# Optimization experiments

Hardware: AMD Instinct MI355X
Metric: run time of the kernel (lower is better)

Reference implementation:

```python
import jax, jax.numpy as jnp
import numpy as np

B, T, HID = 2, 2048, 2048
NH, NKV, HD = 16, 4, 128
GROUPS = NH // NKV

def _rotate_half(t):
    t1, t2 = jnp.split(t, 2, axis=-1)
    return jnp.concatenate([-t2, t1], axis=-1)

def _apply_rotary(t, cos, sin):
    # t: [B, H, T, D], cos/sin: [1, 1, T, D]
    return t * cos + _rotate_half(t) * sin

def setup_inputs() -> dict:
    key = jax.random.key(0)
    ks = jax.random.split(key, 6)
    x = jax.random.normal(ks[0], (B, T, HID), dtype=jnp.float32)
    # real rotary tables
    inv_freq = 1.0 / (10000.0 ** (jnp.arange(0, HD, 2, dtype=jnp.float32) / HD))
    pos = jnp.arange(T, dtype=jnp.float32)
    freqs = jnp.outer(pos, inv_freq)            # [T, D/2]
    emb = jnp.concatenate([freqs, freqs], -1)   # [T, D]
    cos = jnp.cos(emb)[None, None]              # [1,1,T,D]
    sin = jnp.sin(emb)[None, None]
    s = 0.02
    Wq = jax.random.normal(ks[1], (HID, NH * HD), dtype=jnp.float32) * s
    Wk = jax.random.normal(ks[2], (HID, NKV * HD), dtype=jnp.float32) * s
    Wv = jax.random.normal(ks[3], (HID, NKV * HD), dtype=jnp.float32) * s
    Wo = jax.random.normal(ks[4], (NH * HD, HID), dtype=jnp.float32) * s
    return {"x": x, "cos": cos, "sin": sin, "Wq": Wq, "Wk": Wk, "Wv": Wv, "Wo": Wo}

def reference(x, cos, sin, Wq, Wk, Wv, Wo):
    b, t, _ = x.shape
    q = (x @ Wq).reshape(b, t, NH, HD).transpose(0, 2, 1, 3)    # [B,NH,T,D]
    k = (x @ Wk).reshape(b, t, NKV, HD).transpose(0, 2, 1, 3)   # [B,NKV,T,D]
    v = (x @ Wv).reshape(b, t, NKV, HD).transpose(0, 2, 1, 3)
    q = _apply_rotary(q, cos, sin)
    k = _apply_rotary(k, cos, sin)
    # GQA without repeat_interleave: group q-heads by kv-head
    qg = q.reshape(b, NKV, GROUPS, t, HD)                       # [B,KV,G,T,D]
    scale = 1.0 / jnp.sqrt(jnp.float32(HD))
    scores = jnp.einsum('bkgtd,bksd->bkgts', qg, k) * scale     # [B,KV,G,T,S]
    causal = jnp.tril(jnp.ones((t, t), dtype=bool))
    scores = jnp.where(causal[None, None, None], scores, jnp.float32(-1e30))
    attn = jax.nn.softmax(scores, axis=-1)
    out = jnp.einsum('bkgts,bksd->bkgtd', attn, v)              # [B,KV,G,T,D]
    out = out.reshape(b, NH, t, HD).transpose(0, 2, 1, 3).reshape(b, t, NH * HD)
    return out @ Wo
```

## Files before the change

kernel.cpp:

```cpp
#include <hip/hip_runtime.h>
#include <hip/hip_bf16.h>
#include <cstdint>

typedef unsigned short u16;
typedef unsigned int u32;
typedef __bf16 bf16x8 __attribute__((ext_vector_type(8)));
typedef float f32x4 __attribute__((ext_vector_type(4)));

#define BDIM 2
#define TDIM 2048
#define HIDDIM 2048
#define NHEAD 16
#define NKVH 4
#define HD 128
#define MROWS (BDIM*TDIM)
#define NQKV 3072
#define KDIM 2048

#define MFMA16(a,b,c) __builtin_amdgcn_mfma_f32_16x16x32_bf16((a),(b),(c),0,0,0)

__device__ __forceinline__ u16 f2bf(float f) {
    __bf16 h = (__bf16)f;
    return __builtin_bit_cast(u16, h);
}
__device__ __forceinline__ float bf2f(u32 u) {
    u <<= 16;
    return __builtin_bit_cast(float, u);
}
__device__ __forceinline__ void gld16(const void* g, void* l) {
    __builtin_amdgcn_global_load_lds(
        (const __attribute__((address_space(1))) u32*)g,
        (__attribute__((address_space(3))) u32*)l, 16, 0, 0);
}

__global__ __launch_bounds__(256) void prep_kernel(const float* __restrict__ x,
                                                   u16* __restrict__ xb,
                                                   const float* __restrict__ Wq,
                                                   const float* __restrict__ Wk,
                                                   const float* __restrict__ Wv,
                                                   const float* __restrict__ Wo,
                                                   u16* __restrict__ Wqkvt,
                                                   u16* __restrict__ Wot) {
    __shared__ float tile[32][33];
    const int bi = blockIdx.x;
    const int tid = threadIdx.x;
    if (bi < 4096) {
        size_t i = ((size_t)bi * 256 + tid) * 8;
        float4 a = *(const float4*)(x + i);
        float4 b = *(const float4*)(x + i + 4);
        uint4 v;
        v.x = (u32)f2bf(a.x) | ((u32)f2bf(a.y) << 16);
        v.y = (u32)f2bf(a.z) | ((u32)f2bf(a.w) << 16);
        v.z = (u32)f2bf(b.x) | ((u32)f2bf(b.y) << 16);
        v.w = (u32)f2bf(b.z) | ((u32)f2bf(b.w) << 16);
        *(uint4*)(xb + i) = v;
        return;
    }
    const float* src;
    u16* dst;
    int N, n0, k0;
    if (bi < 8192) {
        int t = bi - 4096; src = Wq; dst = Wqkvt; N = 2048;
        n0 = (t & 63) * 32; k0 = (t >> 6) * 32;
    } else if (bi < 9216) {
        int t = bi - 8192; src = Wk; dst = Wqkvt + (size_t)2048 * KDIM; N = 512;
        n0 = (t & 15) * 32; k0 = (t >> 4) * 32;
    } else if (bi < 10240) {
        int t = bi - 9216; src = Wv; dst = Wqkvt + (size_t)2560 * KDIM; N = 512;
        n0 = (t & 15) * 32; k0 = (t >> 4) * 32;
    } else {
        int t = bi - 10240; src = Wo; dst = Wot; N = 2048;
        n0 = (t & 63) * 32; k0 = (t >> 6) * 32;
    }
    const int tx = tid & 31, ty = tid >> 5;
#pragma unroll
    for (int r = 0; r < 4; r++)
        tile[ty + 8*r][tx] = src[(size_t)(k0 + ty + 8*r) * N + n0 + tx];
    __syncthreads();
#pragma unroll
    for (int r = 0; r < 4; r++)
        dst[(size_t)(n0 + ty + 8*r) * KDIM + k0 + tx] = f2bf(tile[tx][ty + 8*r]);
}

template<int OUT_BF16>
__global__ void __launch_bounds__(256, 2) gemm_bt(const u16* __restrict__ A,
                                                  const u16* __restrict__ Bt,
                                                  void* __restrict__ C, int ldc) {
    __shared__ __align__(16) u16 Al[128 * 32];
    __shared__ __align__(16) u16 Bl[128 * 32];
    const int tid = threadIdx.x;
    const int lane = tid & 63;
    const int w = tid >> 6;
    const int wm = (w & 1) * 64;
    const int wn = (w >> 1) * 64;
    const int quad = lane >> 4;
    const int l15 = lane & 15;
    const size_t bm = (size_t)blockIdx.x * 128;
    const size_t bn = (size_t)blockIdx.y * 128;

    const int srow = lane >> 2;
    const int kq = (lane & 3) ^ ((lane >> 3) & 3);
    const int i0 = 2 * w, i1 = 2 * w + 1;

    const u16* ga0 = A + (bm + i0*16 + srow) * KDIM + kq * 8;
    const u16* ga1 = A + (bm + i1*16 + srow) * KDIM + kq * 8;
    const u16* gb0 = Bt + (bn + i0*16 + srow) * KDIM + kq * 8;
    const u16* gb1 = Bt + (bn + i1*16 + srow) * KDIM + kq * 8;

    const int swz = ((quad ^ ((l15 >> 1) & 3)) << 3);
    int aoff[4], boff[4];
#pragma unroll
    for (int t = 0; t < 4; t++) {
        aoff[t] = (wm + t*16 + l15) * 32 + swz;
        boff[t] = (wn + t*16 + l15) * 32 + swz;
    }

    f32x4 acc[4][4] = {};

    for (int kt = 0; kt < KDIM / 32; kt++) {
        gld16(ga0 + kt*32, &Al[i0 * 512]);
        gld16(ga1 + kt*32, &Al[i1 * 512]);
        gld16(gb0 + kt*32, &Bl[i0 * 512]);
        gld16(gb1 + kt*32, &Bl[i1 * 512]);
        __syncthreads();
        bf16x8 af[4], bfv[4];
#pragma unroll
        for (int t = 0; t < 4; t++) {
            af[t]  = *(const bf16x8*)&Al[aoff[t]];
            bfv[t] = *(const bf16x8*)&Bl[boff[t]];
        }
#pragma unroll
        for (int mt = 0; mt < 4; mt++)
#pragma unroll
            for (int nt = 0; nt < 4; nt++)
                acc[mt][nt] = MFMA16(af[mt], bfv[nt], acc[mt][nt]);
        __syncthreads();
    }

#pragma unroll
    for (int mt = 0; mt < 4; mt++) {
        size_t m0 = bm + wm + mt*16 + quad*4;
#pragma unroll
        for (int nt = 0; nt < 4; nt++) {
            size_t n = bn + wn + nt*16 + l15;
#pragma unroll
            for (int r = 0; r < 4; r++) {
                if (OUT_BF16)
                    ((u16*)C)[(m0 + r) * (size_t)ldc + n] = f2bf(acc[mt][nt][r]);
                else
                    ((float*)C)[(m0 + r) * (size_t)ldc + n] = acc[mt][nt][r];
            }
        }
    }
}

__global__ __launch_bounds__(256) void rotary_kernel(u16* __restrict__ QKV,
                                                     const float* __restrict__ cosT,
                                                     const float* __restrict__ sinT) {
    int i = blockIdx.x * 256 + threadIdx.x;
    int m = i / 320;
    int rem = i - m * 320;
    int head = rem >> 4;
    int d0 = (rem & 15) << 2;
    int t = m & (TDIM - 1);
    int col;
    float sc;
    if (head < NHEAD) {
        col = head * HD + d0;
        sc = 0.08838834764831845f * 1.4426950408889634f;
    } else {
        col = HIDDIM + (head - NHEAD) * HD + d0;
        sc = 1.0f;
    }
    u16* p0 = QKV + (size_t)m * NQKV + col;
    u16* p1 = p0 + 64;
    float4 cv = *(const float4*)(cosT + t * HD + d0);
    float4 sv = *(const float4*)(sinT + t * HD + d0);
    uint2 qa = *(const uint2*)p0;
    uint2 qb = *(const uint2*)p1;
    float f0[4] = { bf2f(qa.x & 0xffffu), bf2f(qa.x >> 16), bf2f(qa.y & 0xffffu), bf2f(qa.y >> 16) };
    float f1[4] = { bf2f(qb.x & 0xffffu), bf2f(qb.x >> 16), bf2f(qb.y & 0xffffu), bf2f(qb.y >> 16) };
    float c[4] = { cv.x, cv.y, cv.z, cv.w };
    float s[4] = { sv.x, sv.y, sv.z, sv.w };
    u16 o0[4], o1[4];
#pragma unroll
    for (int k = 0; k < 4; k++) {
        o0[k] = f2bf((f0[k] * c[k] - f1[k] * s[k]) * sc);
        o1[k] = f2bf((f1[k] * c[k] + f0[k] * s[k]) * sc);
    }
    uint2 w0, w1;
    w0.x = (u32)o0[0] | ((u32)o0[1] << 16);
    w0.y = (u32)o0[2] | ((u32)o0[3] << 16);
    w1.x = (u32)o1[0] | ((u32)o1[1] << 16);
    w1.y = (u32)o1[2] | ((u32)o1[3] << 16);
    *(uint2*)p0 = w0;
    *(uint2*)p1 = w1;
}

__global__ void __launch_bounds__(256, 2) attn_kernel(const u16* __restrict__ QKV,
                                                      u16* __restrict__ AO) {
    constexpr int LV = 72;
    __shared__ __align__(16) u16 Kl[2][64 * 128];
    __shared__ __align__(16) u16 Vt[128 * LV];

    const int pa = blockIdx.x;
    const int h  = blockIdx.y;
    const int b  = blockIdx.z;
    const int kh = h >> 2;
    const int tid = threadIdx.x;
    const int lane = tid & 63;
    const int w = tid >> 6;
    const int quad = lane >> 4;
    const int l15 = lane & 15;

    const size_t rowbase = (size_t)b * TDIM;
    const u16* Qb = QKV + rowbase * NQKV + h * HD;
    const u16* Kb = QKV + rowbase * NQKV + HIDDIM + kh * HD;
    const u16* Vb = Kb + NKVH * HD;

    int krow[4], kgch[4];
#pragma unroll
    for (int i = 0; i < 4; i++) {
        krow[i] = w*16 + i*4 + quad;
        kgch[i] = l15 ^ (krow[i] & 7);
    }
    const int sp0 = tid & 31, dch0 = tid >> 5, dch1 = dch0 + 8;
    const int s0v = sp0 * 2;
    const int ccv = (s0v & ~0x1C) | ((s0v & 0x0C) << 1) | ((s0v & 0x10) >> 2);

#pragma unroll 1
    for (int ph = 0; ph < 2; ph++) {
        const int qt = ph ? (31 - pa) : pa;

        bf16x8 qf[4];
        {
            const u16* qr = Qb + (size_t)(qt*64 + w*16 + l15) * NQKV;
#pragma unroll
            for (int kt = 0; kt < 4; kt++)
                qf[kt] = *(const bf16x8*)(qr + kt*32 + quad*8);
        }
        f32x4 O[8] = {};
        float mrun = -1e30f, lrun = 0.0f;

#pragma unroll
        for (int i = 0; i < 4; i++)
            gld16(Kb + (size_t)krow[i] * NQKV + kgch[i]*8, &Kl[0][(w*16 + i*4) * 128]);
        uint4 vr0a, vr0b, vr1a, vr1b;
        {
            const u16* g0 = Vb + (size_t)s0v * NQKV + dch0*8;
            vr0a = *(const uint4*)g0;
            vr0b = *(const uint4*)(g0 + NQKV);
            const u16* g1 = Vb + (size_t)s0v * NQKV + dch1*8;
            vr1a = *(const uint4*)g1;
            vr1b = *(const uint4*)(g1 + NQKV);
        }

#pragma unroll 1
        for (int j = 0; j <= qt; j++) {
            {
                u32 ra[4] = { vr0a.x, vr0a.y, vr0a.z, vr0a.w };
                u32 rb[4] = { vr0b.x, vr0b.y, vr0b.z, vr0b.w };
                int d0 = dch0*8;
#pragma unroll
                for (int k2 = 0; k2 < 4; k2++) {
                    u32 lo = (ra[k2] & 0xffffu) | (rb[k2] << 16);
                    u32 hi = (ra[k2] >> 16) | (rb[k2] & 0xffff0000u);
                    *(u32*)&Vt[(d0 + 2*k2)     * LV + ccv] = lo;
                    *(u32*)&Vt[(d0 + 2*k2 + 1) * LV + ccv] = hi;
                }
                u32 rc[4] = { vr1a.x, vr1a.y, vr1a.z, vr1a.w };
                u32 rd[4] = { vr1b.x, vr1b.y, vr1b.z, vr1b.w };
                d0 = dch1*8;
#pragma unroll
                for (int k2 = 0; k2 < 4; k2++) {
                    u32 lo = (rc[k2] & 0xffffu) | (rd[k2] << 16);
                    u32 hi = (rc[k2] >> 16) | (rd[k2] & 0xffff0000u);
                    *(u32*)&Vt[(d0 + 2*k2)     * LV + ccv] = lo;
                    *(u32*)&Vt[(d0 + 2*k2 + 1) * LV + ccv] = hi;
                }
            }
            __syncthreads();

            if (j < qt) {
                const u16* Kbn = Kb + (size_t)(j+1) * 64 * NQKV;
                u16* kl = Kl[(j+1) & 1];
#pragma unroll
                for (int i = 0; i < 4; i++)
                    gld16(Kbn + (size_t)krow[i] * NQKV + kgch[i]*8, &kl[(w*16 + i*4) * 128]);
                const u16* Vbn = Vb + (size_t)(j+1) * 64 * NQKV;
                const u16* g0 = Vbn + (size_t)s0v * NQKV + dch0*8;
                vr0a = *(const uint4*)g0;
                vr0b = *(const uint4*)(g0 + NQKV);
                const u16* g1 = Vbn + (size_t)s0v * NQKV + dch1*8;
                vr1a = *(const uint4*)g1;
                vr1b = *(const uint4*)(g1 + NQKV);
            }

            const u16* kl = Kl[j & 1];
            f32x4 S[4] = {};
            __builtin_amdgcn_s_setprio(1);
#pragma unroll
            for (int kt = 0; kt < 4; kt++) {
                int p = (kt*4 + quad) ^ (l15 & 7);
#pragma unroll
                for (int nt = 0; nt < 4; nt++) {
                    bf16x8 afr = *(const bf16x8*)&kl[(nt*16 + l15)*128 + p*8];
                    S[nt] = MFMA16(afr, qf[kt], S[nt]);
                }
            }
            __builtin_amdgcn_s_setprio(0);

            if (j == qt) {
                const int qloc = w*16 + l15;
#pragma unroll
                for (int nt = 0; nt < 4; nt++) {
                    const int sb = nt*16 + quad*4;
#pragma unroll
                    for (int r = 0; r < 4; r++)
                        if (sb + r > qloc) S[nt][r] = -1e30f;
                }
            }

            bool grow;
            {
                float mx0 = fmaxf(fmaxf(S[0][0], S[0][1]), fmaxf(S[0][2], S[0][3]));
                float mx1 = fmaxf(fmaxf(S[1][0], S[1][1]), fmaxf(S[1][2], S[1][3]));
                float mx2 = fmaxf(fmaxf(S[2][0], S[2][1]), fmaxf(S[2][2], S[2][3]));
                float mx3 = fmaxf(fmaxf(S[3][0], S[3][1]), fmaxf(S[3][2], S[3][3]));
                float mx = fmaxf(fmaxf(mx0, mx1), fmaxf(mx2, mx3));
                mx = fmaxf(mx, __shfl_xor(mx, 16, 64));
                mx = fmaxf(mx, __shfl_xor(mx, 32, 64));
                grow = __any(mx > mrun + 8.0f);
                float alpha = 1.0f;
                if (grow) {
                    float mnew = fmaxf(mrun, mx);
                    alpha = __builtin_amdgcn_exp2f(mrun - mnew);
                    mrun = mnew;
                }
                float rs = 0.0f;
#pragma unroll
                for (int nt = 0; nt < 4; nt++)
#pragma unroll
                    for (int r = 0; r < 4; r++) {
                        float pv = __builtin_amdgcn_exp2f(S[nt][r] - mrun);
                        S[nt][r] = pv;
                        rs += pv;
                    }
                rs += __shfl_xor(rs, 16, 64);
                rs += __shfl_xor(rs, 32, 64);
                lrun = lrun * alpha + rs;
                if (grow) {
#pragma unroll
                    for (int nt = 0; nt < 8; nt++)
                        O[nt] *= alpha;
                }
            }

            u32 c0[4], c1[4];
#pragma unroll
            for (int nt = 0; nt < 4; nt++) {
                c0[nt] = (u32)f2bf(S[nt][0]) | ((u32)f2bf(S[nt][1]) << 16);
                c1[nt] = (u32)f2bf(S[nt][2]) | ((u32)f2bf(S[nt][3]) << 16);
            }
            __builtin_amdgcn_s_setprio(1);
#pragma unroll
            for (int kt = 0; kt < 2; kt++) {
                uint4 bq;
                bq.x = c0[2*kt];
                bq.y = c1[2*kt];
                bq.z = c0[2*kt+1];
                bq.w = c1[2*kt+1];
                bf16x8 pf = __builtin_bit_cast(bf16x8, bq);
#pragma unroll
                for (int nt = 0; nt < 8; nt++) {
                    bf16x8 av = *(const bf16x8*)&Vt[(nt*16 + l15) * LV + kt*32 + quad*8];
                    O[nt] = MFMA16(av, pf, O[nt]);
                }
            }
            __builtin_amdgcn_s_setprio(0);
            __syncthreads();
        }

        {
            float inv = 1.0f / lrun;
            size_t row = rowbase + qt*64 + w*16 + l15;
            u16* outp = AO + row * HIDDIM + h * HD + quad*4;
#pragma unroll
            for (int nt = 0; nt < 8; nt++) {
                uint2 o;
                o.x = (u32)f2bf(O[nt][0] * inv) | ((u32)f2bf(O[nt][1] * inv) << 16);
                o.y = (u32)f2bf(O[nt][2] * inv) | ((u32)f2bf(O[nt][3] * inv) << 16);
                *(uint2*)(outp + nt*16) = o;
            }
        }
    }
}

extern "C" void kernel_launch(void* const* d_in, const int* in_sizes, int n_in,
                              void* d_out, int out_size, void* d_ws, size_t ws_size,
                              hipStream_t stream) {
    (void)in_sizes; (void)n_in; (void)out_size; (void)ws_size;
    const float* x    = (const float*)d_in[0];
    const float* cosT = (const float*)d_in[1];
    const float* sinT = (const float*)d_in[2];
    const float* Wq   = (const float*)d_in[3];
    const float* Wk   = (const float*)d_in[4];
    const float* Wv   = (const float*)d_in[5];
    const float* Wo   = (const float*)d_in[6];

    char* ws = (char*)d_ws;
    u16* QKV   = (u16*)ws;
    u16* xb    = (u16*)(ws + (size_t)MROWS * NQKV * 2);
    u16* Wqkvt = (u16*)(ws + (size_t)MROWS * NQKV * 2 + (size_t)MROWS * HIDDIM * 2);
    u16* Wot   = Wqkvt + (size_t)NQKV * KDIM;

    prep_kernel<<<14336, 256, 0, stream>>>(x, xb, Wq, Wk, Wv, Wo, Wqkvt, Wot);
    gemm_bt<1><<<dim3(32, 24), 256, 0, stream>>>(xb, Wqkvt, QKV, NQKV);
    rotary_kernel<<<5120, 256, 0, stream>>>(QKV, cosT, sinT);
    attn_kernel<<<dim3(16, 16, 2), 256, 0, stream>>>(QKV, xb);
    gemm_bt<0><<<dim3(32, 16), 256, 0, stream>>>(xb, Wot, d_out, HIDDIM);
}
```

Baseline: 307.2 us.

## Double-buffer transposed V tile to drop one barrier per KV iteration

The transposed V tile in shared memory becomes double-buffered. The next tile's transpose-and-store now happens after the P·V MFMAs of the current tile rather than at the top of the next iteration. This removes the trailing __syncthreads per KV step, leaving one barrier per iteration, and lets the V scatter overlap other waves' compute. It costs an extra 18KB of LDS, which may reduce occupancy under the 2-blocks-per-CU launch bound. It also requires the K/V prefetch ordering to stay correct with only a single barrier.

```diff
diff --git a/kernel.cpp b/kernel.cpp
--- a/kernel.cpp
+++ b/kernel.cpp
@@ -201,7 +201,7 @@
                                                       u16* __restrict__ AO) {
     constexpr int LV = 72;
     __shared__ __align__(16) u16 Kl[2][64 * 128];
-    __shared__ __align__(16) u16 Vt[128 * LV];
+    __shared__ __align__(16) u16 Vt[2][128 * LV];
 
     const int pa = blockIdx.x;
     const int h  = blockIdx.y;
@@ -242,9 +242,8 @@
         f32x4 O[8] = {};
         float mrun = -1e30f, lrun = 0.0f;
 
-#pragma unroll
-        for (int i = 0; i < 4; i++)
-            gld16(Kb + (size_t)krow[i] * NQKV + kgch[i]*8, &Kl[0][(w*16 + i*4) * 128]);
+        __syncthreads();
+
         uint4 vr0a, vr0b, vr1a, vr1b;
         {
             const u16* g0 = Vb + (size_t)s0v * NQKV + dch0*8;
@@ -254,39 +253,38 @@
             vr1a = *(const uint4*)g1;
             vr1b = *(const uint4*)(g1 + NQKV);
         }
+#pragma unroll
+        for (int i = 0; i < 4; i++)
+            gld16(Kb + (size_t)krow[i] * NQKV + kgch[i]*8, &Kl[0][(w*16 + i*4) * 128]);
+        {
+            u16* vt = &Vt[0][0];
+            u32 ra[4] = { vr0a.x, vr0a.y, vr0a.z, vr0a.w };
+            u32 rb[4] = { vr0b.x, vr0b.y, vr0b.z, vr0b.w };
+            int d0 = dch0*8;
+#pragma unroll
+            for (int k2 = 0; k2 < 4; k2++) {
+                u32 lo = (ra[k2] & 0xffffu) | (rb[k2] << 16);
+                u32 hi = (ra[k2] >> 16) | (rb[k2] & 0xffff0000u);
+                *(u32*)&vt[(d0 + 2*k2)     * LV + ccv] = lo;
+                *(u32*)&vt[(d0 + 2*k2 + 1) * LV + ccv] = hi;
+            }
+            u32 rc[4] = { vr1a.x, vr1a.y, vr1a.z, vr1a.w };
+            u32 rd[4] = { vr1b.x, vr1b.y, vr1b.z, vr1b.w };
+            d0 = dch1*8;
+#pragma unroll
+            for (int k2 = 0; k2 < 4; k2++) {
+                u32 lo = (rc[k2] & 0xffffu) | (rd[k2] << 16);
+                u32 hi = (rc[k2] >> 16) | (rd[k2] & 0xffff0000u);
+                *(u32*)&vt[(d0 + 2*k2)     * LV + ccv] = lo;
+                *(u32*)&vt[(d0 + 2*k2 + 1) * LV + ccv] = hi;
+            }
+        }
 
 #pragma unroll 1
         for (int j = 0; j <= qt; j++) {
-            {
-                u32 ra[4] = { vr0a.x, vr0a.y, vr0a.z, vr0a.w };
-                u32 rb[4] = { vr0b.x, vr0b.y, vr0b.z, vr0b.w };
-                int d0 = dch0*8;
-#pragma unroll
-                for (int k2 = 0; k2 < 4; k2++) {
-                    u32 lo = (ra[k2] & 0xffffu) | (rb[k2] << 16);
-                    u32 hi = (ra[k2] >> 16) | (rb[k2] & 0xffff0000u);
-                    *(u32*)&Vt[(d0 + 2*k2)     * LV + ccv] = lo;
-                    *(u32*)&Vt[(d0 + 2*k2 + 1) * LV + ccv] = hi;
-                }
-                u32 rc[4] = { vr1a.x, vr1a.y, vr1a.z, vr1a.w };
-                u32 rd[4] = { vr1b.x, vr1b.y, vr1b.z, vr1b.w };
-                d0 = dch1*8;
-#pragma unroll
-                for (int k2 = 0; k2 < 4; k2++) {
-                    u32 lo = (rc[k2] & 0xffffu) | (rd[k2] << 16);
-                    u32 hi = (rc[k2] >> 16) | (rd[k2] & 0xffff0000u);
-                    *(u32*)&Vt[(d0 + 2*k2)     * LV + ccv] = lo;
-                    *(u32*)&Vt[(d0 + 2*k2 + 1) * LV + ccv] = hi;
-                }
-            }
             __syncthreads();
 
             if (j < qt) {
-                const u16* Kbn = Kb + (size_t)(j+1) * 64 * NQKV;
-                u16* kl = Kl[(j+1) & 1];
-#pragma unroll
-                for (int i = 0; i < 4; i++)
-                    gld16(Kbn + (size_t)krow[i] * NQKV + kgch[i]*8, &kl[(w*16 + i*4) * 128]);
                 const u16* Vbn = Vb + (size_t)(j+1) * 64 * NQKV;
                 const u16* g0 = Vbn + (size_t)s0v * NQKV + dch0*8;
                 vr0a = *(const uint4*)g0;
@@ -294,9 +292,14 @@
                 const u16* g1 = Vbn + (size_t)s0v * NQKV + dch1*8;
                 vr1a = *(const uint4*)g1;
                 vr1b = *(const uint4*)(g1 + NQKV);
-            }
-
-            const u16* kl = Kl[j & 1];
+                const u16* Kbn = Kb + (size_t)(j+1) * 64 * NQKV;
+                u16* kl = &Kl[(j+1) & 1][0];
+#pragma unroll
+                for (int i = 0; i < 4; i++)
+                    gld16(Kbn + (size_t)krow[i] * NQKV + kgch[i]*8, &kl[(w*16 + i*4) * 128]);
+            }
+
+            const u16* kl = &Kl[j & 1][0];
             f32x4 S[4] = {};
             __builtin_amdgcn_s_setprio(1);
 #pragma unroll
@@ -362,6 +365,7 @@
                 c0[nt] = (u32)f2bf(S[nt][0]) | ((u32)f2bf(S[nt][1]) << 16);
                 c1[nt] = (u32)f2bf(S[nt][2]) | ((u32)f2bf(S[nt][3]) << 16);
             }
+            const u16* vt = &Vt[j & 1][0];
             __builtin_amdgcn_s_setprio(1);
 #pragma unroll
             for (int kt = 0; kt < 2; kt++) {
@@ -373,12 +377,35 @@
                 bf16x8 pf = __builtin_bit_cast(bf16x8, bq);
 #pragma unroll
                 for (int nt = 0; nt < 8; nt++) {
-                    bf16x8 av = *(const bf16x8*)&Vt[(nt*16 + l15) * LV + kt*32 + quad*8];
+                    bf16x8 av = *(const bf16x8*)&vt[(nt*16 + l15) * LV + kt*32 + quad*8];
                     O[nt] = MFMA16(av, pf, O[nt]);
                 }
             }
             __builtin_amdgcn_s_setprio(0);
-            __syncthreads();
+
+            if (j < qt) {
+                u16* vtn = &Vt[(j+1) & 1][0];
+                u32 ra[4] = { vr0a.x, vr0a.y, vr0a.z, vr0a.w };
+                u32 rb[4] = { vr0b.x, vr0b.y, vr0b.z, vr0b.w };
+                int d0 = dch0*8;
+#pragma unroll
+                for (int k2 = 0; k2 < 4; k2++) {
+                    u32 lo = (ra[k2] & 0xffffu) | (rb[k2] << 16);
+                    u32 hi = (ra[k2] >> 16) | (rb[k2] & 0xffff0000u);
+                    *(u32*)&vtn[(d0 + 2*k2)     * LV + ccv] = lo;
+                    *(u32*)&vtn[(d0 + 2*k2 + 1) * LV + ccv] = hi;
+                }
+                u32 rc[4] = { vr1a.x, vr1a.y, vr1a.z, vr1a.w };
+                u32 rd[4] = { vr1b.x, vr1b.y, vr1b.z, vr1b.w };
+                d0 = dch1*8;
+#pragma unroll
+                for (int k2 = 0; k2 < 4; k2++) {
+                    u32 lo = (rc[k2] & 0xffffu) | (rd[k2] << 16);
+                    u32 hi = (rc[k2] >> 16) | (rd[k2] & 0xffff0000u);
+                    *(u32*)&vtn[(d0 + 2*k2)     * LV + ccv] = lo;
+                    *(u32*)&vtn[(d0 + 2*k2 + 1) * LV + ccv] = hi;
+                }
+            }
         }
 
         {
```

Measured after the change: 303.4 us. Within noise of the previous version (-1.2%).

## Process 128 query rows per attention block, reusing K/V tiles across two sub-tiles

Applied to the files above, without the earlier changes.

Each attention block now handles a 128-row query tile (two 16-row sub-tiles per wave) instead of two paired 64-row tiles, so every K/V tile staged in shared memory feeds twice as many MFMAs. The grid becomes a flat 512-block launch, ordered so that long and short causal tiles are interleaved for load balance. This is meant to halve K/V global loads and the V transpose work per query row and to raise MFMA density. In exchange, register pressure roughly doubles for the accumulators and Q fragments, which may reduce occupancy, and per-block work becomes more uneven.

```diff
diff --git a/kernel.cpp b/kernel.cpp
--- a/kernel.cpp
+++ b/kernel.cpp
@@ -203,9 +203,14 @@
     __shared__ __align__(16) u16 Kl[2][64 * 128];
     __shared__ __align__(16) u16 Vt[128 * LV];
 
-    const int pa = blockIdx.x;
-    const int h  = blockIdx.y;
-    const int b  = blockIdx.z;
+    const int l  = blockIdx.x;
+    const int cc = l & 255;
+    const int pq = cc & 7;
+    const int h  = (cc >> 3) & 15;
+    const int b  = cc >> 7;
+    const int qt = (l >> 8) ? (15 - pq) : pq;
+    const int nj = 2 * qt + 2;
+
     const int kh = h >> 2;
     const int tid = threadIdx.x;
     const int lane = tid & 63;
@@ -228,170 +233,188 @@
     const int s0v = sp0 * 2;
     const int ccv = (s0v & ~0x1C) | ((s0v & 0x0C) << 1) | ((s0v & 0x10) >> 2);
 
+    bf16x8 qf[2][4];
+#pragma unroll
+    for (int mi = 0; mi < 2; mi++) {
+        const u16* qr = Qb + (size_t)(qt*128 + w*32 + mi*16 + l15) * NQKV;
+#pragma unroll
+        for (int kt = 0; kt < 4; kt++)
+            qf[mi][kt] = *(const bf16x8*)(qr + kt*32 + quad*8);
+    }
+    f32x4 O[2][8] = {};
+    float mrun[2] = { -1e30f, -1e30f }, lrun[2] = { 0.0f, 0.0f };
+
+#pragma unroll
+    for (int i = 0; i < 4; i++)
+        gld16(Kb + (size_t)krow[i] * NQKV + kgch[i]*8, &Kl[0][(w*16 + i*4) * 128]);
+    uint4 vr0a, vr0b, vr1a, vr1b;
+    {
+        const u16* g0 = Vb + (size_t)s0v * NQKV + dch0*8;
+        vr0a = *(const uint4*)g0;
+        vr0b = *(const uint4*)(g0 + NQKV);
+        const u16* g1 = Vb + (size_t)s0v * NQKV + dch1*8;
+        vr1a = *(const uint4*)g1;
+        vr1b = *(const uint4*)(g1 + NQKV);
+    }
+
 #pragma unroll 1
-    for (int ph = 0; ph < 2; ph++) {
-        const int qt = ph ? (31 - pa) : pa;
-
-        bf16x8 qf[4];
+    for (int j = 0; j < nj; j++) {
         {
-            const u16* qr = Qb + (size_t)(qt*64 + w*16 + l15) * NQKV;
-#pragma unroll
-            for (int kt = 0; kt < 4; kt++)
-                qf[kt] = *(const bf16x8*)(qr + kt*32 + quad*8);
-        }
-        f32x4 O[8] = {};
-        float mrun = -1e30f, lrun = 0.0f;
-
-#pragma unroll
-        for (int i = 0; i < 4; i++)
-            gld16(Kb + (size_t)krow[i] * NQKV + kgch[i]*8, &Kl[0][(w*16 + i*4) * 128]);
-        uint4 vr0a, vr0b, vr1a, vr1b;
-        {
-            const u16* g0 = Vb + (size_t)s0v * NQKV + dch0*8;
+            u32 ra[4] = { vr0a.x, vr0a.y, vr0a.z, vr0a.w };
+            u32 rb[4] = { vr0b.x, vr0b.y, vr0b.z, vr0b.w };
+            int d0 = dch0*8;
+#pragma unroll
+            for (int k2 = 0; k2 < 4; k2++) {
+                u32 lo = (ra[k2] & 0xffffu) | (rb[k2] << 16);
+                u32 hi = (ra[k2] >> 16) | (rb[k2] & 0xffff0000u);
+                *(u32*)&Vt[(d0 + 2*k2)     * LV + ccv] = lo;
+                *(u32*)&Vt[(d0 + 2*k2 + 1) * LV + ccv] = hi;
+            }
+            u32 rc[4] = { vr1a.x, vr1a.y, vr1a.z, vr1a.w };
+            u32 rd[4] = { vr1b.x, vr1b.y, vr1b.z, vr1b.w };
+            d0 = dch1*8;
+#pragma unroll
+            for (int k2 = 0; k2 < 4; k2++) {
+                u32 lo = (rc[k2] & 0xffffu) | (rd[k2] << 16);
+                u32 hi = (rc[k2] >> 16) | (rd[k2] & 0xffff0000u);
+                *(u32*)&Vt[(d0 + 2*k2)     * LV + ccv] = lo;
+                *(u32*)&Vt[(d0 + 2*k2 + 1) * LV + ccv] = hi;
+            }
+        }
+        __syncthreads();
+
+        if (j + 1 < nj) {
+            const u16* Kbn = Kb + (size_t)(j+1) * 64 * NQKV;
+            u16* kl = &Kl[(j+1) & 1][0];
+#pragma unroll
+            for (int i = 0; i < 4; i++)
+                gld16(Kbn + (size_t)krow[i] * NQKV + kgch[i]*8, &kl[(w*16 + i*4) * 128]);
+            const u16* Vbn = Vb + (size_t)(j+1) * 64 * NQKV;
+            const u16* g0 = Vbn + (size_t)s0v * NQKV + dch0*8;
             vr0a = *(const uint4*)g0;
             vr0b = *(const uint4*)(g0 + NQKV);
-            const u16* g1 = Vb + (size_t)s0v * NQKV + dch1*8;
+            const u16* g1 = Vbn + (size_t)s0v * NQKV + dch1*8;
             vr1a = *(const uint4*)g1;
             vr1b = *(const uint4*)(g1 + NQKV);
         }
 
-#pragma unroll 1
-        for (int j = 0; j <= qt; j++) {
-            {
-                u32 ra[4] = { vr0a.x, vr0a.y, vr0a.z, vr0a.w };
-                u32 rb[4] = { vr0b.x, vr0b.y, vr0b.z, vr0b.w };
-                int d0 = dch0*8;
-#pragma unroll
-                for (int k2 = 0; k2 < 4; k2++) {
-                    u32 lo = (ra[k2] & 0xffffu) | (rb[k2] << 16);
-                    u32 hi = (ra[k2] >> 16) | (rb[k2] & 0xffff0000u);
-                    *(u32*)&Vt[(d0 + 2*k2)     * LV + ccv] = lo;
-                    *(u32*)&Vt[(d0 + 2*k2 + 1) * LV + ccv] = hi;
+        const u16* kl = &Kl[j & 1][0];
+        f32x4 S[2][4] = {};
+        __builtin_amdgcn_s_setprio(1);
+#pragma unroll
+        for (int kt = 0; kt < 4; kt++) {
+            int p = (kt*4 + quad) ^ (l15 & 7);
+#pragma unroll
+            for (int nt = 0; nt < 4; nt++) {
+                bf16x8 afr = *(const bf16x8*)&kl[(nt*16 + l15)*128 + p*8];
+                S[0][nt] = MFMA16(afr, qf[0][kt], S[0][nt]);
+                S[1][nt] = MFMA16(afr, qf[1][kt], S[1][nt]);
+            }
+        }
+        __builtin_amdgcn_s_setprio(0);
+
+        if (j >= 2*qt) {
+            const int sb0 = (j - 2*qt) * 64;
+#pragma unroll
+            for (int mi = 0; mi < 2; mi++) {
+                const int qloc = w*32 + mi*16 + l15;
+#pragma unroll
+                for (int nt = 0; nt < 4; nt++) {
+                    const int sb = sb0 + nt*16 + quad*4;
+#pragma unroll
+                    for (int r = 0; r < 4; r++)
+                        if (sb + r > qloc) S[mi][nt][r] = -1e30f;
                 }
-                u32 rc[4] = { vr1a.x, vr1a.y, vr1a.z, vr1a.w };
-                u32 rd[4] = { vr1b.x, vr1b.y, vr1b.z, vr1b.w };
-                d0 = dch1*8;
-#pragma unroll
-                for (int k2 = 0; k2 < 4; k2++) {
-                    u32 lo = (rc[k2] & 0xffffu) | (rd[k2] << 16);
-                    u32 hi = (rc[k2] >> 16) | (rd[k2] & 0xffff0000u);
-                    *(u32*)&Vt[(d0 + 2*k2)     * LV + ccv] = lo;
-                    *(u32*)&Vt[(d0 + 2*k2 + 1) * LV + ccv] = hi;
+            }
+        }
+
+        {
+            float mx[2];
+#pragma unroll
+            for (int mi = 0; mi < 2; mi++) {
+                float a0 = fmaxf(fmaxf(S[mi][0][0], S[mi][0][1]), fmaxf(S[mi][0][2], S[mi][0][3]));
+                float a1 = fmaxf(fmaxf(S[mi][1][0], S[mi][1][1]), fmaxf(S[mi][1][2], S[mi][1][3]));
+                float a2 = fmaxf(fmaxf(S[mi][2][0], S[mi][2][1]), fmaxf(S[mi][2][2], S[mi][2][3]));
+                float a3 = fmaxf(fmaxf(S[mi][3][0], S[mi][3][1]), fmaxf(S[mi][3][2], S[mi][3][3]));
+                float m = fmaxf(fmaxf(a0, a1), fmaxf(a2, a3));
+                m = fmaxf(m, __shfl_xor(m, 16, 64));
+                m = fmaxf(m, __shfl_xor(m, 32, 64));
+                mx[mi] = m;
+            }
+            bool grow = __any((mx[0] > mrun[0] + 8.0f) | (mx[1] > mrun[1] + 8.0f));
+            float alpha[2] = { 1.0f, 1.0f };
+            if (grow) {
+#pragma unroll
+                for (int mi = 0; mi < 2; mi++) {
+                    float mn = fmaxf(mrun[mi], mx[mi]);
+                    alpha[mi] = __builtin_amdgcn_exp2f(mrun[mi] - mn);
+                    mrun[mi] = mn;
                 }
             }
-            __syncthreads();
-
-            if (j < qt) {
-                const u16* Kbn = Kb + (size_t)(j+1) * 64 * NQKV;
-                u16* kl = Kl[(j+1) & 1];
-#pragma unroll
-                for (int i = 0; i < 4; i++)
-                    gld16(Kbn + (size_t)krow[i] * NQKV + kgch[i]*8, &kl[(w*16 + i*4) * 128]);
-                const u16* Vbn = Vb + (size_t)(j+1) * 64 * NQKV;
-                const u16* g0 = Vbn + (size_t)s0v * NQKV + dch0*8;
-                vr0a = *(const uint4*)g0;
-                vr0b = *(const uint4*)(g0 + NQKV);
-                const u16* g1 = Vbn + (size_t)s0v * NQKV + dch1*8;
-                vr1a = *(const uint4*)g1;
-                vr1b = *(const uint4*)(g1 + NQKV);
-            }
-
-            const u16* kl = Kl[j & 1];
-            f32x4 S[4] = {};
-            __builtin_amdgcn_s_setprio(1);
-#pragma unroll
-            for (int kt = 0; kt < 4; kt++) {
-                int p = (kt*4 + quad) ^ (l15 & 7);
-#pragma unroll
-                for (int nt = 0; nt < 4; nt++) {
-                    bf16x8 afr = *(const bf16x8*)&kl[(nt*16 + l15)*128 + p*8];
-                    S[nt] = MFMA16(afr, qf[kt], S[nt]);
-                }
-            }
-            __builtin_amdgcn_s_setprio(0);
-
-            if (j == qt) {
-                const int qloc = w*16 + l15;
-#pragma unroll
-                for (int nt = 0; nt < 4; nt++) {
-                    const int sb = nt*16 + quad*4;
-#pragma unroll
-                    for (int r = 0; r < 4; r++)
-                        if (sb + r > qloc) S[nt][r] = -1e30f;
-                }
-            }
-
-            bool grow;
-            {
-                float mx0 = fmaxf(fmaxf(S[0][0], S[0][1]), fmaxf(S[0][2], S[0][3]));
-                float mx1 = fmaxf(fmaxf(S[1][0], S[1][1]), fmaxf(S[1][2], S[1][3]));
-                float mx2 = fmaxf(fmaxf(S[2][0], S[2][1]), fmaxf(S[2][2], S[2][3]));
-                float mx3 = fmaxf(fmaxf(S[3][0], S[3][1]), fmaxf(S[3][2], S[3][3]));
-                float mx = fmaxf(fmaxf(mx0, mx1), fmaxf(mx2, mx3));
-                mx = fmaxf(mx, __shfl_xor(mx, 16, 64));
-                mx = fmaxf(mx, __shfl_xor(mx, 32, 64));
-                grow = __any(mx > mrun + 8.0f);
-                float alpha = 1.0f;
-                if (grow) {
-                    float mnew = fmaxf(mrun, mx);
-                    alpha = __builtin_amdgcn_exp2f(mrun - mnew);
-                    mrun = mnew;
-                }
+#pragma unroll
+            for (int mi = 0; mi < 2; mi++) {
                 float rs = 0.0f;
 #pragma unroll
                 for (int nt = 0; nt < 4; nt++)
 #pragma unroll
                     for (int r = 0; r < 4; r++) {
-                        float pv = __builtin_amdgcn_exp2f(S[nt][r] - mrun);
-                        S[nt][r] = pv;
+                        float pv = __builtin_amdgcn_exp2f(S[mi][nt][r] - mrun[mi]);
+                        S[mi][nt][r] = pv;
                         rs += pv;
                     }
                 rs += __shfl_xor(rs, 16, 64);
                 rs += __shfl_xor(rs, 32, 64);
-                lrun = lrun * alpha + rs;
-                if (grow) {
+                lrun[mi] = lrun[mi] * alpha[mi] + rs;
+            }
+            if (grow) {
+#pragma unroll
+                for (int mi = 0; mi < 2; mi++)
 #pragma unroll
                     for (int nt = 0; nt < 8; nt++)
-                        O[nt] *= alpha;
-                }
-            }
-
-            u32 c0[4], c1[4];
+                        O[mi][nt] *= alpha[mi];
+            }
+        }
+
+        u32 c0[2][4], c1[2][4];
+#pragma unroll
+        for (int mi = 0; mi < 2; mi++)
 #pragma unroll
             for (int nt = 0; nt < 4; nt++) {
-                c0[nt] = (u32)f2bf(S[nt][0]) | ((u32)f2bf(S[nt][1]) << 16);
-                c1[nt] = (u32)f2bf(S[nt][2]) | ((u32)f2bf(S[nt][3]) << 16);
-            }
-            __builtin_amdgcn_s_setprio(1);
-#pragma unroll
-            for (int kt = 0; kt < 2; kt++) {
-                uint4 bq;
-                bq.x = c0[2*kt];
-                bq.y = c1[2*kt];
-                bq.z = c0[2*kt+1];
-                bq.w = c1[2*kt+1];
-                bf16x8 pf = __builtin_bit_cast(bf16x8, bq);
-#pragma unroll
-                for (int nt = 0; nt < 8; nt++) {
-                    bf16x8 av = *(const bf16x8*)&Vt[(nt*16 + l15) * LV + kt*32 + quad*8];
-                    O[nt] = MFMA16(av, pf, O[nt]);
-                }
-            }
-            __builtin_amdgcn_s_setprio(0);
-            __syncthreads();
-        }
-
-        {
-            float inv = 1.0f / lrun;
-            size_t row = rowbase + qt*64 + w*16 + l15;
-            u16* outp = AO + row * HIDDIM + h * HD + quad*4;
+                c0[mi][nt] = (u32)f2bf(S[mi][nt][0]) | ((u32)f2bf(S[mi][nt][1]) << 16);
+                c1[mi][nt] = (u32)f2bf(S[mi][nt][2]) | ((u32)f2bf(S[mi][nt][3]) << 16);
+            }
+        __builtin_amdgcn_s_setprio(1);
+#pragma unroll
+        for (int kt = 0; kt < 2; kt++) {
+            uint4 b0, b1;
+            b0.x = c0[0][2*kt];   b0.y = c1[0][2*kt];
+            b0.z = c0[0][2*kt+1]; b0.w = c1[0][2*kt+1];
+            b1.x = c0[1][2*kt];   b1.y = c1[1][2*kt];
+            b1.z = c0[1][2*kt+1]; b1.w = c1[1][2*kt+1];
+            bf16x8 pf0 = __builtin_bit_cast(bf16x8, b0);
+            bf16x8 pf1 = __builtin_bit_cast(bf16x8, b1);
 #pragma unroll
             for (int nt = 0; nt < 8; nt++) {
-                uint2 o;
-                o.x = (u32)f2bf(O[nt][0] * inv) | ((u32)f2bf(O[nt][1] * inv) << 16);
-                o.y = (u32)f2bf(O[nt][2] * inv) | ((u32)f2bf(O[nt][3] * inv) << 16);
-                *(uint2*)(outp + nt*16) = o;
-            }
+                bf16x8 av = *(const bf16x8*)&Vt[(nt*16 + l15) * LV + kt*32 + quad*8];
+                O[0][nt] = MFMA16(av, pf0, O[0][nt]);
+                O[1][nt] = MFMA16(av, pf1, O[1][nt]);
+            }
+        }
+        __builtin_amdgcn_s_setprio(0);
+        __syncthreads();
+    }
+
+#pragma unroll
+    for (int mi = 0; mi < 2; mi++) {
+        float inv = 1.0f / lrun[mi];
+        size_t row = rowbase + qt*128 + w*32 + mi*16 + l15;
+        u16* outp = AO + row * HIDDIM + h * HD + quad*4;
+#pragma unroll
+        for (int nt = 0; nt < 8; nt++) {
+            uint2 o;
+            o.x = (u32)f2bf(O[mi][nt][0] * inv) | ((u32)f2bf(O[mi][nt][1] * inv) << 16);
+            o.y = (u32)f2bf(O[mi][nt][2] * inv) | ((u32)f2bf(O[mi][nt][3] * inv) << 16);
+            *(uint2*)(outp + nt*16) = o;
         }
     }
 }
@@ -417,6 +440,6 @@
     prep_kernel<<<14336, 256, 0, stream>>>(x, xb, Wq, Wk, Wv, Wo, Wqkvt, Wot);
     gemm_bt<1><<<dim3(32, 24), 256, 0, stream>>>(xb, Wqkvt, QKV, NQKV);
     rotary_kernel<<<5120, 256, 0, stream>>>(QKV, cosT, sinT);
-    attn_kernel<<<dim3(16, 16, 2), 256, 0, stream>>>(QKV, xb);
+    attn_kernel<<<512, 256, 0, stream>>>(QKV, xb);
     gemm_bt<0><<<dim3(32, 16), 256, 0, stream>>>(xb, Wot, d_out, HIDDIM);
 }
```

New measurement: 312.7 us. About the same (+1.8%).
